# Performance work log

Measured on AMD Instinct MI355X. Metric: run time of the kernel, lower is better.

The kernel has to match this reference:

```python
import jax, jax.numpy as jnp
import numpy as np

N = 20000      # nodes
E = 320000     # edges
GD = 256       # g_dim
H = 8          # head_n
D = 32         # head_d
XD = 256       # x_dim
PS = 4         # x_ps
HID = 512      # FF hidden (hardcoded in module)
EPS = 1e-5
SCALE = GD ** -0.5  # note: module scales by g_dim**-0.5, not head_d**-0.5


def layernorm(x, w, b):
    mu = jnp.mean(x, axis=-1, keepdims=True)
    var = jnp.var(x, axis=-1, keepdims=True)
    return (x - mu) * jax.lax.rsqrt(var + EPS) * w + b


def setup_inputs() -> dict:
    key = jax.random.key(0)
    ks = jax.random.split(key, 16)
    inp = {
        "x": jax.random.normal(ks[0], (N, XD, PS, PS), jnp.float32),
        "h": jax.random.normal(ks[1], (N, GD), jnp.float32),
        "src": jax.random.randint(ks[2], (E,), 0, N, jnp.int32),
        "dst": jax.random.randint(ks[3], (E,), 0, N, jnp.int32),
        # xproj conv (kernel covers full patch -> equivalent to a linear)
        "conv_w": jax.random.normal(ks[4], (GD, XD, PS, PS), jnp.float32) * 0.02,
        "conv_b": jnp.zeros((GD,), jnp.float32),
        # GraphT outer LayerNorm
        "norm_w": jnp.ones((GD,), jnp.float32),
        "norm_b": jnp.zeros((GD,), jnp.float32),
        # attention norm_in + projections
        "nin_w": jnp.ones((GD,), jnp.float32),
        "nin_b": jnp.zeros((GD,), jnp.float32),
        "w_qkv": jax.random.normal(ks[5], (3 * H * D, GD), jnp.float32) * 0.02,
        "w_out": jax.random.normal(ks[6], (GD, H * D), jnp.float32) * 0.02,
        "b_out": jnp.zeros((GD,), jnp.float32),
        # FeedForward: LayerNorm + Linear(GD,HID) + GELU + Linear(HID,GD)
        "ffn_w": jnp.ones((GD,), jnp.float32),
        "ffn_b": jnp.zeros((GD,), jnp.float32),
        "w1": jax.random.normal(ks[7], (HID, GD), jnp.float32) * 0.02,
        "b1": jnp.zeros((HID,), jnp.float32),
        "w2": jax.random.normal(ks[8], (GD, HID), jnp.float32) * 0.02,
        "b2": jnp.zeros((GD,), jnp.float32),
    }
    return inp


def reference(x, h, src, dst, conv_w, conv_b, norm_w, norm_b, nin_w, nin_b,
              w_qkv, w_out, b_out, ffn_w, ffn_b, w1, b1, w2, b2):
    # xproj: Conv2d with kernel == full spatial extent -> linear over flattened patch
    xp = x.reshape(N, XD * PS * PS) @ conv_w.reshape(GD, XD * PS * PS).T + conv_b  # [N, GD]

    hn = layernorm(h, norm_w, norm_b)  # GraphT.norm

    # --- GraphAttention ---
    s = layernorm(hn, nin_w, nin_b)                    # norm_in
    qkv = s @ w_qkv.T                                  # [N, 3*H*D]
    q, k, v = jnp.split(qkv, 3, axis=-1)
    q = q.reshape(N, H, D)
    k = k.reshape(N, H, D)
    v = v.reshape(N, H, D)

    # per-edge elementwise attention (DGL u_mul_v), scaled
    att = q[src] * k[dst] * SCALE                      # [E, H, D]
    # edge softmax over incoming edges of each destination, per (h, d) slot
    amax = jax.ops.segment_max(att, dst, num_segments=N)   # [N, H, D]
    e = jnp.exp(att - amax[dst])
    z = jax.ops.segment_sum(e, dst, num_segments=N)
    a = e / z[dst]                                     # [E, H, D]
    # weighted aggregation: sum over edges of v_src * att
    rst = jax.ops.segment_sum(v[src] * a, dst, num_segments=N)  # [N, H, D]

    attn_out = rst.reshape(N, H * D) @ w_out.T + b_out  # to_out (dropout=eval noop)

    # --- FeedForward (norm -> linear -> gelu -> linear) ---
    f = layernorm(attn_out, ffn_w, ffn_b)
    f = jax.nn.gelu(f @ w1.T + b1, approximate=False)
    f = f @ w2.T + b2

    out = f + hn + xp
    return out
```

## Files before the change

kernel.cpp:

```cpp
#include <hip/hip_runtime.h>
#include <hip/hip_bf16.h>
#include <math.h>

typedef __hip_bfloat16 bf16;
typedef __attribute__((ext_vector_type(8))) short bf16x8;
typedef __attribute__((ext_vector_type(4))) float f32x4;

#define N_NODES 20000
#define N_EDGES 320000
#define GD 256
#define HID 512
#define QKV3 768
#define SCALE 0.0625f
#define EPS 1e-5f

__device__ __forceinline__ float b2f(bf16 x) { return __bfloat162float(x); }
__device__ __forceinline__ bf16 f2b(float x) { return __float2bfloat16(x); }
__device__ __forceinline__ short f2bs(float x) {
    bf16 b = __float2bfloat16(x);
    union { bf16 b; short s; } u; u.b = b; return u.s;
}
__device__ __forceinline__ float ldf(const void* p, size_t i, int isbf) {
    return isbf ? __bfloat162float(((const bf16*)p)[i]) : ((const float*)p)[i];
}

__global__ void detect_kernel(const void* __restrict__ normw, int* __restrict__ flag) {
    if (threadIdx.x == 0) {
        unsigned short u = ((const unsigned short*)normw)[0];
        *flag = (u == 0x3F80) ? 1 : 0;
    }
}

__global__ void conv_bf16_kernel(const void* __restrict__ in, bf16* __restrict__ out,
                                 int n, const int* __restrict__ flag) {
    int i = blockIdx.x * 256 + threadIdx.x;
    int fl = *flag;
    if (i < n) out[i] = f2b(ldf(in, i, fl));
}

__global__ void count_kernel(const int* __restrict__ dst, int* __restrict__ deg) {
    int e = blockIdx.x * 256 + threadIdx.x;
    if (e < N_EDGES) atomicAdd(&deg[dst[e]], 1);
}

__global__ void scan_kernel(const int* __restrict__ deg, int* __restrict__ offsets,
                            int* __restrict__ cursor) {
    const int T = 1024;
    int t = threadIdx.x;
    int chunk = (N_NODES + T - 1) / T;
    int beg = t * chunk;
    int end = beg + chunk; if (end > N_NODES) end = N_NODES;
    int s = 0;
    for (int i = beg; i < end; ++i) s += deg[i];
    __shared__ int ls[T];
    ls[t] = s;
    __syncthreads();
    for (int off = 1; off < T; off <<= 1) {
        int v = (t >= off) ? ls[t - off] : 0;
        __syncthreads();
        ls[t] += v;
        __syncthreads();
    }
    int run = (t == 0) ? 0 : ls[t - 1];
    for (int i = beg; i < end; ++i) {
        offsets[i] = run; cursor[i] = run; run += deg[i];
    }
    if (t == T - 1) offsets[N_NODES] = run;
}

__global__ void fill_kernel(const int* __restrict__ src, const int* __restrict__ dst,
                            int* __restrict__ cursor, int* __restrict__ ssrc) {
    int e = blockIdx.x * 256 + threadIdx.x;
    if (e < N_EDGES) {
        int p = atomicAdd(&cursor[dst[e]], 1);
        ssrc[p] = src[e];
    }
}

__global__ void ln_fused_kernel(const void* __restrict__ h,
                                const void* __restrict__ nw, const void* __restrict__ nb,
                                const void* __restrict__ iw, const void* __restrict__ ib,
                                float* __restrict__ hn, bf16* __restrict__ s,
                                const int* __restrict__ flag) {
    int wave = threadIdx.x >> 6, lane = threadIdx.x & 63;
    int n = blockIdx.x * 4 + wave;
    int fl = *flag;
    size_t base = (size_t)n * GD;
    float x[4]; float sum = 0.f, sq = 0.f;
    #pragma unroll
    for (int i = 0; i < 4; ++i) {
        x[i] = ldf(h, base + lane + 64 * i, fl);
        sum += x[i]; sq += x[i] * x[i];
    }
    #pragma unroll
    for (int off = 32; off; off >>= 1) { sum += __shfl_xor(sum, off); sq += __shfl_xor(sq, off); }
    float mu = sum * (1.0f / GD);
    float rs = rsqrtf(sq * (1.0f / GD) - mu * mu + EPS);
    float y[4]; float s2 = 0.f, q2 = 0.f;
    #pragma unroll
    for (int i = 0; i < 4; ++i) {
        int j = lane + 64 * i;
        y[i] = (x[i] - mu) * rs * ldf(nw, j, fl) + ldf(nb, j, fl);
        hn[base + j] = y[i];
        s2 += y[i]; q2 += y[i] * y[i];
    }
    #pragma unroll
    for (int off = 32; off; off >>= 1) { s2 += __shfl_xor(s2, off); q2 += __shfl_xor(q2, off); }
    float mu2 = s2 * (1.0f / GD);
    float rs2 = rsqrtf(q2 * (1.0f / GD) - mu2 * mu2 + EPS);
    #pragma unroll
    for (int i = 0; i < 4; ++i) {
        int j = lane + 64 * i;
        s[base + j] = f2b((y[i] - mu2) * rs2 * ldf(iw, j, fl) + ldf(ib, j, fl));
    }
}

__global__ void ln_kernel(const bf16* __restrict__ in,
                          const void* __restrict__ w, const void* __restrict__ b,
                          bf16* __restrict__ out, const int* __restrict__ flag) {
    int wave = threadIdx.x >> 6, lane = threadIdx.x & 63;
    int n = blockIdx.x * 4 + wave;
    int fl = *flag;
    size_t base = (size_t)n * GD;
    float x[4]; float sum = 0.f, sq = 0.f;
    #pragma unroll
    for (int i = 0; i < 4; ++i) {
        x[i] = b2f(in[base + lane + 64 * i]);
        sum += x[i]; sq += x[i] * x[i];
    }
    #pragma unroll
    for (int off = 32; off; off >>= 1) { sum += __shfl_xor(sum, off); sq += __shfl_xor(sq, off); }
    float mu = sum * (1.0f / GD);
    float rs = rsqrtf(sq * (1.0f / GD) - mu * mu + EPS);
    #pragma unroll
    for (int i = 0; i < 4; ++i) {
        int j = lane + 64 * i;
        out[base + j] = f2b((x[i] - mu) * rs * ldf(w, j, fl) + ldf(b, j, fl));
    }
}

__global__ void attn_kernel(const bf16* __restrict__ qkv, const int* __restrict__ offsets,
                            const int* __restrict__ ssrc, bf16* __restrict__ rst) {
    int n = blockIdx.x;
    int j = threadIdx.x;
    float kj = b2f(qkv[(size_t)n * QKV3 + GD + j]) * SCALE;
    int beg = offsets[n], end = offsets[n + 1];
    float m = -INFINITY, l = 0.f, acc = 0.f;
    for (int e = beg; e < end; ++e) {
        int sI = ssrc[e];
        const bf16* qrow = qkv + (size_t)sI * QKV3;
        float a = b2f(qrow[j]) * kj;
        float vv = b2f(qrow[2 * GD + j]);
        float mn = fmaxf(m, a);
        float c = __expf(m - mn);
        float p = __expf(a - mn);
        l = l * c + p;
        acc = acc * c + p * vv;
        m = mn;
    }
    rst[(size_t)n * GD + j] = f2b(end > beg ? acc / l : 0.f);
}

template<int EPI, int DYNA>
__launch_bounds__(256)
__global__ void gemm_bt(const void* __restrict__ A, const bf16* __restrict__ B,
                        const void* __restrict__ bias, void* __restrict__ Cout,
                        const float* __restrict__ add0, const float* __restrict__ add1,
                        int M, int Nn, int K, const int* __restrict__ flag) {
    constexpr int BM = 128, BN = 128, BK = 64, LDW = BK + 8;
    __shared__ bf16 As[BM * LDW];
    __shared__ bf16 Bs[BN * LDW];
    const int m0 = blockIdx.x * BM;
    const int n0 = blockIdx.y * BN;
    const int tid = threadIdx.x;
    const int lane = tid & 63;
    const int wave = tid >> 6;
    const int quad = lane >> 4;
    const int l16 = lane & 15;
    const int wm = (wave & 1) * 64;
    const int wn = (wave >> 1) * 64;
    const int fl = *flag;

    f32x4 acc[4][4] = {};

    for (int k0 = 0; k0 < K; k0 += BK) {
        #pragma unroll
        for (int p = 0; p < 4; ++p) {
            int l = p * 256 + tid;
            int row = l >> 3;
            int ko = (l & 7) * 8;
            int gr = m0 + row; gr = gr < M ? gr : M - 1;
            if (!DYNA || fl) {
                *(int4*)(&As[row * LDW + ko]) =
                    *(const int4*)((const bf16*)A + (size_t)gr * K + k0 + ko);
            } else {
                const float* Af = (const float*)A + (size_t)gr * K + k0 + ko;
                float4 lo = *(const float4*)(Af);
                float4 hi = *(const float4*)(Af + 4);
                bf16x8 v;
                v[0] = f2bs(lo.x); v[1] = f2bs(lo.y); v[2] = f2bs(lo.z); v[3] = f2bs(lo.w);
                v[4] = f2bs(hi.x); v[5] = f2bs(hi.y); v[6] = f2bs(hi.z); v[7] = f2bs(hi.w);
                *(bf16x8*)(&As[row * LDW + ko]) = v;
            }
            *(int4*)(&Bs[row * LDW + ko]) = *(const int4*)(B + (size_t)(n0 + row) * K + k0 + ko);
        }
        __syncthreads();
        #pragma unroll
        for (int kk = 0; kk < BK; kk += 32) {
            bf16x8 af[4], bfm[4];
            #pragma unroll
            for (int i = 0; i < 4; ++i)
                af[i] = *(const bf16x8*)(&As[(wm + i * 16 + l16) * LDW + kk + quad * 8]);
            #pragma unroll
            for (int j = 0; j < 4; ++j)
                bfm[j] = *(const bf16x8*)(&Bs[(wn + j * 16 + l16) * LDW + kk + quad * 8]);
            #pragma unroll
            for (int i = 0; i < 4; ++i)
                #pragma unroll
                for (int j = 0; j < 4; ++j)
                    acc[i][j] = __builtin_amdgcn_mfma_f32_16x16x32_bf16(af[i], bfm[j], acc[i][j], 0, 0, 0);
        }
        __syncthreads();
    }

    #pragma unroll
    for (int i = 0; i < 4; ++i) {
        #pragma unroll
        for (int j = 0; j < 4; ++j) {
            int col = n0 + wn + j * 16 + l16;
            float bv = bias ? ldf(bias, col, fl) : 0.0f;
            #pragma unroll
            for (int r = 0; r < 4; ++r) {
                int gr = m0 + wm + i * 16 + quad * 4 + r;
                if (gr >= M) continue;
                float v = acc[i][j][r] + bv;
                size_t idx = (size_t)gr * Nn + col;
                if (EPI == 2) v = 0.5f * v * (1.0f + erff(v * 0.70710678118f));
                if (EPI == 3) v += add0[idx] + add1[idx];
                if (EPI == 0)      ((float*)Cout)[idx] = v;
                else if (EPI == 3) { if (fl) ((bf16*)Cout)[idx] = f2b(v); else ((float*)Cout)[idx] = v; }
                else               ((bf16*)Cout)[idx] = f2b(v);
            }
        }
    }
}

extern "C" void kernel_launch(void* const* d_in, const int* in_sizes, int n_in,
                              void* d_out, int out_size, void* d_ws, size_t ws_size,
                              hipStream_t stream) {
    const void* x      = d_in[0];
    const void* h      = d_in[1];
    const int*  src    = (const int*)d_in[2];
    const int*  dst    = (const int*)d_in[3];
    const void* conv_w = d_in[4];
    const void* conv_b = d_in[5];
    const void* norm_w = d_in[6];
    const void* norm_b = d_in[7];
    const void* nin_w  = d_in[8];
    const void* nin_b  = d_in[9];
    const void* w_qkv  = d_in[10];
    const void* w_out  = d_in[11];
    const void* b_out  = d_in[12];
    const void* ffn_w  = d_in[13];
    const void* ffn_b  = d_in[14];
    const void* w1     = d_in[15];
    const void* b1     = d_in[16];
    const void* w2     = d_in[17];
    const void* b2     = d_in[18];

    char* w = (char*)d_ws;
    float* xp   = (float*)w; w += (size_t)N_NODES * GD * 4;
    float* hn   = (float*)w; w += (size_t)N_NODES * GD * 4;
    bf16*  s    = (bf16*)w;  w += (size_t)N_NODES * GD * 2;
    bf16*  qkv  = (bf16*)w;  w += (size_t)N_NODES * QKV3 * 2;
    bf16*  rst  = (bf16*)w;  w += (size_t)N_NODES * GD * 2;
    bf16*  attn = (bf16*)w;  w += (size_t)N_NODES * GD * 2;
    bf16*  cw    = (bf16*)w; w += (size_t)4096 * 256 * 2;
    bf16*  wqkvb = (bf16*)w; w += (size_t)768 * 256 * 2;
    bf16*  woutb = (bf16*)w; w += (size_t)256 * 256 * 2;
    bf16*  w1b   = (bf16*)w; w += (size_t)512 * 256 * 2;
    bf16*  w2b   = (bf16*)w; w += (size_t)256 * 512 * 2;
    int* deg     = (int*)w;  w += (size_t)N_NODES * 4;
    int* cursor  = (int*)w;  w += (size_t)N_NODES * 4;
    int* offsets = (int*)w;  w += (size_t)(N_NODES + 4) * 4;
    int* ssrc    = (int*)w;  w += (size_t)N_EDGES * 4;
    int* flag    = (int*)w;  w += 16;
    bf16* fln = s;
    bf16* f1  = qkv;

    detect_kernel<<<1, 64, 0, stream>>>(norm_w, flag);
    conv_bf16_kernel<<<(4096 * 256 + 255) / 256, 256, 0, stream>>>(conv_w, cw, 4096 * 256, flag);
    conv_bf16_kernel<<<(768 * 256 + 255) / 256, 256, 0, stream>>>(w_qkv, wqkvb, 768 * 256, flag);
    conv_bf16_kernel<<<(256 * 256 + 255) / 256, 256, 0, stream>>>(w_out, woutb, 256 * 256, flag);
    conv_bf16_kernel<<<(512 * 256 + 255) / 256, 256, 0, stream>>>(w1, w1b, 512 * 256, flag);
    conv_bf16_kernel<<<(256 * 512 + 255) / 256, 256, 0, stream>>>(w2, w2b, 256 * 512, flag);

    hipMemsetAsync(deg, 0, N_NODES * sizeof(int), stream);
    count_kernel<<<(N_EDGES + 255) / 256, 256, 0, stream>>>(dst, deg);
    scan_kernel<<<1, 1024, 0, stream>>>(deg, offsets, cursor);
    fill_kernel<<<(N_EDGES + 255) / 256, 256, 0, stream>>>(src, dst, cursor, ssrc);

    ln_fused_kernel<<<N_NODES / 4, 256, 0, stream>>>(h, norm_w, norm_b, nin_w, nin_b, hn, s, flag);

    dim3 blk(256);
    gemm_bt<0, 1><<<dim3(157, 2), blk, 0, stream>>>(x, cw, conv_b, xp, nullptr, nullptr, N_NODES, GD, 4096, flag);
    gemm_bt<1, 0><<<dim3(157, 6), blk, 0, stream>>>(s, wqkvb, nullptr, qkv, nullptr, nullptr, N_NODES, QKV3, GD, flag);
    attn_kernel<<<N_NODES, 256, 0, stream>>>(qkv, offsets, ssrc, rst);
    gemm_bt<1, 0><<<dim3(157, 2), blk, 0, stream>>>(rst, woutb, b_out, attn, nullptr, nullptr, N_NODES, GD, GD, flag);
    ln_kernel<<<N_NODES / 4, 256, 0, stream>>>(attn, ffn_w, ffn_b, fln, flag);
    gemm_bt<2, 0><<<dim3(157, 4), blk, 0, stream>>>(fln, w1b, b1, f1, nullptr, nullptr, N_NODES, HID, GD, flag);
    gemm_bt<3, 0><<<dim3(157, 2), blk, 0, stream>>>(f1, w2b, b2, d_out, xp, hn, N_NODES, GD, HID, flag);
}
```

Before: 974.7 us.

## Split-K the conv projection GEMM with atomics and batch weight conversions

The large xproj GEMM (K=4096) is split four ways along K via gridDim.z, with each slice atomically adding its fp32 partial into a zeroed output buffer. Only the first slice adds the bias. This raises the grid from 314 blocks to 1256 so the GPU's compute units are better filled, at the cost of a memset and fp32 atomic traffic. Separately, the five weight-to-bf16 conversion launches are merged into one kernel to cut launch overhead.

```diff
diff --git a/kernel.cpp b/kernel.cpp
--- a/kernel.cpp
+++ b/kernel.cpp
@@ -31,11 +31,22 @@
     }
 }
 
-__global__ void conv_bf16_kernel(const void* __restrict__ in, bf16* __restrict__ out,
-                                 int n, const int* __restrict__ flag) {
+struct ConvArgs {
+    const void* src[5];
+    bf16* dst[5];
+    int n[5];
+};
+__global__ void conv_bf16_all(ConvArgs a, const int* __restrict__ flag) {
     int i = blockIdx.x * 256 + threadIdx.x;
     int fl = *flag;
-    if (i < n) out[i] = f2b(ldf(in, i, fl));
+    #pragma unroll
+    for (int s = 0; s < 5; ++s) {
+        if (i < a.n[s]) {
+            a.dst[s][i] = f2b(ldf(a.src[s], i, fl));
+            return;
+        }
+        i -= a.n[s];
+    }
 }
 
 __global__ void count_kernel(const int* __restrict__ dst, int* __restrict__ deg) {
@@ -181,9 +192,13 @@
     const int wn = (wave >> 1) * 64;
     const int fl = *flag;
 
+    const int kc = K / gridDim.z;
+    const int kbeg = blockIdx.z * kc;
+    const int kend = kbeg + kc;
+
     f32x4 acc[4][4] = {};
 
-    for (int k0 = 0; k0 < K; k0 += BK) {
+    for (int k0 = kbeg; k0 < kend; k0 += BK) {
         #pragma unroll
         for (int p = 0; p < 4; ++p) {
             int l = p * 256 + tid;
@@ -229,6 +244,7 @@
         for (int j = 0; j < 4; ++j) {
             int col = n0 + wn + j * 16 + l16;
             float bv = bias ? ldf(bias, col, fl) : 0.0f;
+            if (EPI == 4 && blockIdx.z != 0) bv = 0.0f;
             #pragma unroll
             for (int r = 0; r < 4; ++r) {
                 int gr = m0 + wm + i * 16 + quad * 4 + r;
@@ -239,6 +255,7 @@
                 if (EPI == 3) v += add0[idx] + add1[idx];
                 if (EPI == 0)      ((float*)Cout)[idx] = v;
                 else if (EPI == 3) { if (fl) ((bf16*)Cout)[idx] = f2b(v); else ((float*)Cout)[idx] = v; }
+                else if (EPI == 4) atomicAdd(&((float*)Cout)[idx], v);
                 else               ((bf16*)Cout)[idx] = f2b(v);
             }
         }
@@ -289,11 +306,14 @@
     bf16* f1  = qkv;
 
     detect_kernel<<<1, 64, 0, stream>>>(norm_w, flag);
-    conv_bf16_kernel<<<(4096 * 256 + 255) / 256, 256, 0, stream>>>(conv_w, cw, 4096 * 256, flag);
-    conv_bf16_kernel<<<(768 * 256 + 255) / 256, 256, 0, stream>>>(w_qkv, wqkvb, 768 * 256, flag);
-    conv_bf16_kernel<<<(256 * 256 + 255) / 256, 256, 0, stream>>>(w_out, woutb, 256 * 256, flag);
-    conv_bf16_kernel<<<(512 * 256 + 255) / 256, 256, 0, stream>>>(w1, w1b, 512 * 256, flag);
-    conv_bf16_kernel<<<(256 * 512 + 255) / 256, 256, 0, stream>>>(w2, w2b, 256 * 512, flag);
+    ConvArgs ca;
+    ca.src[0] = conv_w; ca.dst[0] = cw;    ca.n[0] = 4096 * 256;
+    ca.src[1] = w_qkv;  ca.dst[1] = wqkvb; ca.n[1] = 768 * 256;
+    ca.src[2] = w_out;  ca.dst[2] = woutb; ca.n[2] = 256 * 256;
+    ca.src[3] = w1;     ca.dst[3] = w1b;   ca.n[3] = 512 * 256;
+    ca.src[4] = w2;     ca.dst[4] = w2b;   ca.n[4] = 256 * 512;
+    int conv_total = ca.n[0] + ca.n[1] + ca.n[2] + ca.n[3] + ca.n[4];
+    conv_bf16_all<<<(conv_total + 255) / 256, 256, 0, stream>>>(ca, flag);
 
     hipMemsetAsync(deg, 0, N_NODES * sizeof(int), stream);
     count_kernel<<<(N_EDGES + 255) / 256, 256, 0, stream>>>(dst, deg);
@@ -303,7 +323,8 @@
     ln_fused_kernel<<<N_NODES / 4, 256, 0, stream>>>(h, norm_w, norm_b, nin_w, nin_b, hn, s, flag);
 
     dim3 blk(256);
-    gemm_bt<0, 1><<<dim3(157, 2), blk, 0, stream>>>(x, cw, conv_b, xp, nullptr, nullptr, N_NODES, GD, 4096, flag);
+    hipMemsetAsync(xp, 0, (size_t)N_NODES * GD * 4, stream);
+    gemm_bt<4, 1><<<dim3(157, 2, 4), blk, 0, stream>>>(x, cw, conv_b, xp, nullptr, nullptr, N_NODES, GD, 4096, flag);
     gemm_bt<1, 0><<<dim3(157, 6), blk, 0, stream>>>(s, wqkvb, nullptr, qkv, nullptr, nullptr, N_NODES, QKV3, GD, flag);
     attn_kernel<<<N_NODES, 256, 0, stream>>>(qkv, offsets, ssrc, rst);
     gemm_bt<1, 0><<<dim3(157, 2), blk, 0, stream>>>(rst, woutb, b_out, attn, nullptr, nullptr, N_NODES, GD, GD, flag);
```

After: 929.4 us. 4.7% less time.
